# Performance work log

Measured on AMD Instinct MI355X. Metric: run time of the kernel, lower is better.

The kernel has to match this reference:

```python
import jax, jax.numpy as jnp
import numpy as np

N_NODES = 50000
N_EDGES = 800000
EPS = 1e-5

def _xavier(key, shape):
    fan_in, fan_out = shape[1], shape[0]
    lim = float(np.sqrt(6.0 / (fan_in + fan_out)))
    return jax.random.uniform(key, shape, jnp.float32, -lim, lim)

def setup_inputs() -> dict:
    key = jax.random.key(0)
    ks = jax.random.split(key, 12)
    x = jax.random.normal(ks[0], (N_NODES, 166), jnp.float32)
    edge_index = jax.random.randint(ks[1], (2, N_EDGES), 0, N_NODES, jnp.int32)
    dims = [(256, 166), (128, 256), (64, 128)]
    inp = {"x": x, "edge_index": edge_index}
    # SAGEConv layers: lin_l (applied to aggregated neighbors, has bias) and lin_r (self)
    names = ["1", "2", "e"]
    for i, (nm, (do, di)) in enumerate(zip(names, dims)):
        inp[f"Wl{nm}"] = _xavier(ks[2 + 2 * i], (do, di))
        inp[f"Wr{nm}"] = _xavier(ks[3 + 2 * i], (do, di))
        inp[f"b{nm}"] = jnp.zeros((do,), jnp.float32)
    # BatchNorm params for the two hidden conv layers
    inp["g1"] = jnp.ones((256,), jnp.float32); inp["bt1"] = jnp.zeros((256,), jnp.float32)
    inp["g2"] = jnp.ones((128,), jnp.float32); inp["bt2"] = jnp.zeros((128,), jnp.float32)
    # classifier
    inp["Wc"] = _xavier(ks[8], (2, 64))
    inp["bc"] = jnp.zeros((2,), jnp.float32)
    return inp

def _sage_conv(x, src, dst, Wl, Wr, b):
    # mean aggregation of source features at destination nodes
    agg = jax.ops.segment_sum(x[src], dst, num_segments=N_NODES)  # [N, d]
    deg = jax.ops.segment_sum(jnp.ones((src.shape[0],), x.dtype), dst, num_segments=N_NODES)
    agg = agg / jnp.maximum(deg, 1.0)[:, None]
    return agg @ Wl.T + x @ Wr.T + b

def _bn(x, g, b):
    m = jnp.mean(x, axis=0)
    v = jnp.var(x, axis=0)
    return (x - m) * jax.lax.rsqrt(v + EPS) * g + b

def reference(x, edge_index, Wl1, Wr1, b1, Wl2, Wr2, b2, Wle, Wre, be, g1, bt1, g2, bt2, Wc, bc):
    src, dst = edge_index[0], edge_index[1]
    h = _sage_conv(x, src, dst, Wl1, Wr1, b1)
    h = jax.nn.relu(_bn(h, g1, bt1))
    h = _sage_conv(h, src, dst, Wl2, Wr2, b2)
    h = jax.nn.relu(_bn(h, g2, bt2))
    embeddings = _sage_conv(h, src, dst, Wle, Wre, be)  # [N, 64]
    logits = embeddings @ Wc.T + bc  # [N, 2]
    return (logits, embeddings)
```

## Files before the change

kernel.cpp:

```cpp
#include <hip/hip_runtime.h>

#define NN 50000
#define NE 800000
#define NB 256
#define BNODES ((NN + NB - 1) / NB)
#define CAP 4096
#define BPART_BLKS ((NE + 8191) / 8192)
#define PREP_BLKS ((NN * 112 + 255) / 256)
#define PACK_BLKS ((180224 + 255) / 256)
static constexpr float BN_EPS = 1e-5f;

typedef __attribute__((ext_vector_type(8))) short bf16x8;
typedef __attribute__((ext_vector_type(4))) float f32x4;

__device__ inline unsigned short f2bf(float f) {
  unsigned int u = __float_as_uint(f);
  return (unsigned short)((u + 0x7FFFu + ((u >> 16) & 1u)) >> 16);
}
__device__ inline float bf2f(unsigned int h) { return __uint_as_float(h << 16); }
__device__ inline void gl_lds16(const char* g, char* l) {
  __builtin_amdgcn_global_load_lds((const __attribute__((address_space(1))) void*)g,
                                   (__attribute__((address_space(3))) void*)l, 16, 0, 0);
}

__device__ void dev_bpart(int bb, const int* __restrict__ src, const int* __restrict__ dst,
                          int* __restrict__ bcur, uint2* __restrict__ pairs) {
  __shared__ int cnt[NB], lbase[NB], lcur[NB];
  int t = threadIdx.x;
  cnt[t] = 0;
  __syncthreads();
  int e0 = bb * 8192 + t;
#pragma unroll
  for (int i = 0; i < 32; ++i) {
    int e = e0 + i * 256;
    if (e < NE) atomicAdd(&cnt[dst[e] / BNODES], 1);
  }
  __syncthreads();
  lbase[t] = cnt[t] ? (t * CAP + atomicAdd(&bcur[t], cnt[t])) : 0;
  lcur[t] = 0;
  __syncthreads();
#pragma unroll
  for (int i = 0; i < 32; ++i) {
    int e = e0 + i * 256;
    if (e < NE) {
      int d = dst[e];
      int b = d / BNODES;
      int p = atomicAdd(&lcur[b], 1);
      pairs[(size_t)lbase[b] + p] = uint2{(unsigned)src[e], (unsigned)d};
    }
  }
}

__global__ void k_front(const int* __restrict__ src, const int* __restrict__ dst,
                        int* __restrict__ bcur, uint2* __restrict__ pairs,
                        const float* __restrict__ x, unsigned int* __restrict__ xbu,
                        unsigned int* __restrict__ aggX,
                        const float* __restrict__ Wl1, const float* __restrict__ Wr1,
                        const float* __restrict__ Wl2, const float* __restrict__ Wr2,
                        const float* __restrict__ Wle, const float* __restrict__ Wre,
                        unsigned short* __restrict__ w1c, unsigned short* __restrict__ w2s,
                        unsigned short* __restrict__ w3s,
                        float* __restrict__ bnacc) {
  int b = blockIdx.x;
  if (b < BPART_BLKS) {
    dev_bpart(b, src, dst, bcur, pairs);
    return;
  }
  b -= BPART_BLKS;
  if (b < PREP_BLKS) {
    int i = b * 256 + threadIdx.x;
    if (i >= NN * 112) return;
    int r = i / 112, q = i - r * 112;
    if (q < 84) {
      int c0 = 2 * q, c1 = c0 + 1;
      float v0 = (c0 < 166) ? x[(size_t)r * 166 + c0] : 0.f;
      float v1 = (c1 < 166) ? x[(size_t)r * 166 + c1] : 0.f;
      xbu[(size_t)r * 96 + q] = (unsigned)f2bf(v0) | ((unsigned)f2bf(v1) << 16);
    } else if (q < 96) {
      xbu[(size_t)r * 96 + q] = 0u;
    } else if (q < 109) {
      aggX[(size_t)r * 96 + 83 + (q - 96)] = 0u;
    }
    return;
  }
  b -= PREP_BLKS;
  if (b < PACK_BLKS) {
    int idx = b * 256 + threadIdx.x;
    if (idx < 98304) {
      int n = idx / 384, k = idx - n * 384;
      float v = 0.f;
      if (k < 166) v = Wl1[(size_t)n * 166 + k];
      else if (k >= 192 && k < 358) v = Wr1[(size_t)n * 166 + (k - 192)];
      w1c[idx] = f2bf(v);
    } else if (idx < 163840) {
      int j = idx - 98304;
      int n = j / 256, k = j - n * 256;
      w2s[j] = f2bf(n < 128 ? Wl2[(size_t)n * 256 + k] : Wr2[(size_t)(n - 128) * 256 + k]);
    } else if (idx < 180224) {
      int j = idx - 163840;
      int n = j / 128, k = j - n * 128;
      w3s[j] = f2bf(n < 64 ? Wle[(size_t)n * 128 + k] : Wre[(size_t)(n - 64) * 128 + k]);
    }
    return;
  }
  int z = (b - PACK_BLKS) * 256 + threadIdx.x;
  if (z < 1024) bnacc[z] = 0.f;
}

__global__ void k_bscatter(const uint2* __restrict__ pairs, const int* __restrict__ bcur,
                           int2* __restrict__ begend, int* __restrict__ col) {
  __shared__ int dcnt[NB], ts[NB], doff[NB], dcur[NB];
  int t = threadIdx.x;
  int b = blockIdx.x;
  int n0 = b * BNODES;
  int ncnt = min(NN - n0, BNODES);
  int e0 = b * CAP, e1 = e0 + bcur[b];
  dcnt[t] = 0;
  __syncthreads();
  for (int e = e0 + t; e < e1; e += 256) atomicAdd(&dcnt[pairs[e].y - n0], 1);
  __syncthreads();
  ts[t] = dcnt[t];
  __syncthreads();
#pragma unroll
  for (int off = 1; off < NB; off <<= 1) {
    int u = (t >= off) ? ts[t - off] : 0;
    __syncthreads();
    ts[t] += u;
    __syncthreads();
  }
  doff[t] = ts[t] - dcnt[t];
  dcur[t] = 0;
  if (t < ncnt) begend[n0 + t] = int2{e0 + doff[t], e0 + doff[t] + dcnt[t]};
  __syncthreads();
  for (int e = e0 + t; e < e1; e += 256) {
    uint2 pr = pairs[e];
    int ld = pr.y - n0;
    int p = atomicAdd(&dcur[ld], 1);
    col[e0 + doff[ld] + p] = (int)pr.x;
  }
}

template <int D, int U, bool FUSE, bool OUTBF, bool CLS>
__global__ __launch_bounds__(256) void k_aggb(
    const unsigned int* __restrict__ feat, int fsu,
    const int2* __restrict__ begend, const int* __restrict__ col,
    const unsigned int* __restrict__ self, int ssu,
    const float* __restrict__ bias,
    void* __restrict__ outv, int osu,
    const float* __restrict__ Wc, const float* __restrict__ bc,
    float* __restrict__ logits) {
  constexpr int D2 = D / 2;
  constexpr int LPN = (D2 < 64) ? D2 : 64;
  constexpr int NPB = 256 / LPN;
  constexpr int C = (D2 + LPN - 1) / LPN;
  int node = blockIdx.x * NPB + threadIdx.x / LPN;
  if (node >= NN) return;
  int lane = threadIdx.x % LPN;
  int2 be = begend[node];
  int beg = be.x, end = be.y;
  float ax[C], ay[C];
#pragma unroll
  for (int c = 0; c < C; ++c) { ax[c] = 0.f; ay[c] = 0.f; }

  int j = beg;
  for (; j + U <= end; j += U) {
    const unsigned int* fp[U];
#pragma unroll
    for (int u = 0; u < U; ++u) fp[u] = feat + (size_t)col[j + u] * fsu;
#pragma unroll
    for (int c = 0; c < C; ++c) {
      int p = lane + c * LPN;
      unsigned int t[U];
#pragma unroll
      for (int u = 0; u < U; ++u) t[u] = (p < D2) ? fp[u][p] : 0u;
#pragma unroll
      for (int u = 0; u < U; ++u) {
        ax[c] += bf2f(t[u] & 0xffffu);
        ay[c] += bf2f(t[u] >> 16);
      }
    }
  }
  for (; j < end; ++j) {
    const unsigned int* fr = feat + (size_t)col[j] * fsu;
#pragma unroll
    for (int c = 0; c < C; ++c) {
      int p = lane + c * LPN;
      if (p < D2) {
        unsigned int t = fr[p];
        ax[c] += bf2f(t & 0xffffu);
        ay[c] += bf2f(t >> 16);
      }
    }
  }
  float inv = 1.0f / fmaxf((float)(end - beg), 1.0f);
  float s0 = 0.f, s1 = 0.f;
#pragma unroll
  for (int c = 0; c < C; ++c) {
    int p = lane + c * LPN;
    if (p < D2) {
      float vx = ax[c] * inv, vy = ay[c] * inv;
      if constexpr (FUSE) {
        unsigned int s = self[(size_t)node * ssu + p];
        vx += bf2f(s & 0xffffu) + bias[2 * p];
        vy += bf2f(s >> 16) + bias[2 * p + 1];
      }
      if constexpr (OUTBF) {
        unsigned int o = (unsigned int)f2bf(vx) | ((unsigned int)f2bf(vy) << 16);
        ((unsigned int*)outv)[(size_t)node * osu + p] = o;
      } else {
        float2 o{vx, vy};
        *reinterpret_cast<float2*>((float*)outv + (size_t)node * osu + 2 * p) = o;
      }
      if constexpr (CLS) {
        s0 += vx * Wc[2 * p] + vy * Wc[2 * p + 1];
        s1 += vx * Wc[64 + 2 * p] + vy * Wc[64 + 2 * p + 1];
      }
    }
  }
  if constexpr (CLS) {
#pragma unroll
    for (int m = 1; m < LPN; m <<= 1) {
      s0 += __shfl_xor(s0, m);
      s1 += __shfl_xor(s1, m);
    }
    if (lane == 0) {
      logits[node * 2 + 0] = s0 + bc[0];
      logits[node * 2 + 1] = s1 + bc[1];
    }
  }
}

template <bool BIASED, bool STATS>
__global__ __launch_bounds__(256) void k_gemm_mfma(
    const unsigned short* __restrict__ A0, const unsigned short* __restrict__ A1,
    int K1, int Astride, int KC,
    const unsigned short* __restrict__ W,
    const float* __restrict__ bias,
    unsigned short* __restrict__ out, int Ntot,
    float* __restrict__ statacc) {
  __shared__ __align__(16) char lds[65536];
  int tid = threadIdx.x;
  int lane = tid & 63;
  int w = tid >> 6;
  int wr = w >> 1, wc = w & 1;
  int m0 = blockIdx.x * 128;
  int n0 = blockIdx.y * 128;

  int srow = lane >> 3;
  int scol = (lane & 7) << 4;
  int ssw = scol ^ (srow << 4);
  const char* Wb = (const char*)W;

  f32x4 acc[4][4];
#pragma unroll
  for (int i = 0; i < 4; ++i)
#pragma unroll
    for (int j = 0; j < 4; ++j) acc[i][j] = f32x4{0.f, 0.f, 0.f, 0.f};

  auto stage = [&](int buf, int k0) {
    const char* Ab = (const char*)(k0 < K1 ? A0 : A1);
    int koff = k0 < K1 ? k0 : k0 - K1;
    char* dst = lds + buf * 32768 + w * 4096;
#pragma unroll
    for (int i = 0; i < 4; ++i) {
      int row = w * 32 + i * 8 + srow;
      int ga = m0 + row;
      ga = ga < NN ? ga : NN - 1;
      gl_lds16(Ab + ((size_t)ga * Astride + koff) * 2 + ssw, dst + i * 1024);
      gl_lds16(Wb + ((size_t)(n0 + row) * KC + k0) * 2 + ssw, dst + 16384 + i * 1024);
    }
  };
  auto compute = [&](int buf) {
    char* lA = lds + buf * 32768;
    char* lB = lA + 16384;
#pragma unroll
    for (int ks = 0; ks < 2; ++ks) {
      bf16x8 af[4], bfr[4];
      int ac = ks * 64 + ((lane >> 4) << 4);
#pragma unroll
      for (int f = 0; f < 4; ++f) {
        int ar = wr * 64 + f * 16 + (lane & 15);
        af[f] = *reinterpret_cast<const bf16x8*>(lA + ar * 128 + (ac ^ ((ar & 7) << 4)));
        int br = wc * 64 + f * 16 + (lane & 15);
        bfr[f] = *reinterpret_cast<const bf16x8*>(lB + br * 128 + (ac ^ ((br & 7) << 4)));
      }
#pragma unroll
      for (int fm = 0; fm < 4; ++fm)
#pragma unroll
        for (int fn = 0; fn < 4; ++fn)
          acc[fm][fn] = __builtin_amdgcn_mfma_f32_16x16x32_bf16(af[fm], bfr[fn], acc[fm][fn], 0, 0, 0);
    }
  };

  int nt = KC >> 6;
  stage(0, 0);
  if (nt > 1) stage(1, 64);
  for (int t = 0; t < nt - 1; ++t) {
    asm volatile("s_waitcnt vmcnt(8)" ::: "memory");
    __builtin_amdgcn_s_barrier();
    compute(t & 1);
    __builtin_amdgcn_s_barrier();
    if (t + 2 < nt) stage(t & 1, (t + 2) << 6);
  }
  asm volatile("s_waitcnt vmcnt(0)" ::: "memory");
  __builtin_amdgcn_s_barrier();
  compute((nt - 1) & 1);

  int nbase = n0 + wc * 64 + (lane & 15);
  float bv[4] = {0.f, 0.f, 0.f, 0.f};
  if constexpr (BIASED) {
#pragma unroll
    for (int fn = 0; fn < 4; ++fn) bv[fn] = bias[nbase + fn * 16];
  }
  float ssum[4] = {0.f, 0.f, 0.f, 0.f}, sqs[4] = {0.f, 0.f, 0.f, 0.f};
#pragma unroll
  for (int fm = 0; fm < 4; ++fm) {
    int mbase = m0 + wr * 64 + fm * 16 + ((lane >> 4) << 2);
#pragma unroll
    for (int j = 0; j < 4; ++j) {
      int m = mbase + j;
      if (m < NN) {
#pragma unroll
        for (int fn = 0; fn < 4; ++fn) {
          float v = acc[fm][fn][j] + bv[fn];
          out[(size_t)m * Ntot + nbase + fn * 16] = f2bf(v);
          if constexpr (STATS) { ssum[fn] += v; sqs[fn] += v * v; }
        }
      }
    }
  }
  if constexpr (STATS) {
#pragma unroll
    for (int fn = 0; fn < 4; ++fn) {
      float s = ssum[fn], q = sqs[fn];
      s += __shfl_xor(s, 16); s += __shfl_xor(s, 32);
      q += __shfl_xor(q, 16); q += __shfl_xor(q, 32);
      if (lane < 16) {
        atomicAdd(&statacc[nbase + fn * 16], s);
        atomicAdd(&statacc[Ntot + nbase + fn * 16], q);
      }
    }
  }
}

__global__ __launch_bounds__(256) void k_gemm_bn(
    const unsigned short* __restrict__ A, const float* __restrict__ scsh,
    const unsigned short* __restrict__ W,
    unsigned short* __restrict__ out, int KC, int Ntot) {
  __shared__ __align__(16) char lds[65536];
  int tid = threadIdx.x;
  int lane = tid & 63;
  int w = tid >> 6;
  int wr = w >> 1, wc = w & 1;
  int m0 = blockIdx.x * 128;
  int n0 = blockIdx.y * 128;

  int srow = lane >> 3;
  int cb = (lane & 7) << 4;
  int ssw = cb ^ (srow << 4);
  int kk0 = (lane & 7) << 3;
  const char* Wb = (const char*)W;

  f32x4 acc[4][4];
#pragma unroll
  for (int i = 0; i < 4; ++i)
#pragma unroll
    for (int j = 0; j < 4; ++j) acc[i][j] = f32x4{0.f, 0.f, 0.f, 0.f};

  uint4 areg[4];
  float4 sc[4];

  auto loadA = [&](int k0) {
    int kk = k0 + kk0;
    const float4* sp = (const float4*)(scsh + 2 * kk);
    sc[0] = sp[0]; sc[1] = sp[1]; sc[2] = sp[2]; sc[3] = sp[3];
#pragma unroll
    for (int i = 0; i < 4; ++i) {
      int row = w * 32 + i * 8 + srow;
      int ga = m0 + row;
      ga = ga < NN ? ga : NN - 1;
      areg[i] = *reinterpret_cast<const uint4*>(A + (size_t)ga * KC + kk);
    }
  };
  auto writeA = [&](int buf) {
    char* dstb = lds + buf * 32768;
#pragma unroll
    for (int i = 0; i < 4; ++i) {
      int row = w * 32 + i * 8 + srow;
      uint4 v = areg[i], o;
      float a, b;
      a = fmaxf(bf2f(v.x & 0xffffu) * sc[0].x + sc[0].y, 0.f);
      b = fmaxf(bf2f(v.x >> 16)     * sc[0].z + sc[0].w, 0.f);
      o.x = (unsigned)f2bf(a) | ((unsigned)f2bf(b) << 16);
      a = fmaxf(bf2f(v.y & 0xffffu) * sc[1].x + sc[1].y, 0.f);
      b = fmaxf(bf2f(v.y >> 16)     * sc[1].z + sc[1].w, 0.f);
      o.y = (unsigned)f2bf(a) | ((unsigned)f2bf(b) << 16);
      a = fmaxf(bf2f(v.z & 0xffffu) * sc[2].x + sc[2].y, 0.f);
      b = fmaxf(bf2f(v.z >> 16)     * sc[2].z + sc[2].w, 0.f);
      o.z = (unsigned)f2bf(a) | ((unsigned)f2bf(b) << 16);
      a = fmaxf(bf2f(v.w & 0xffffu) * sc[3].x + sc[3].y, 0.f);
      b = fmaxf(bf2f(v.w >> 16)     * sc[3].z + sc[3].w, 0.f);
      o.w = (unsigned)f2bf(a) | ((unsigned)f2bf(b) << 16);
      *reinterpret_cast<uint4*>(dstb + row * 128 + (cb ^ ((row & 7) << 4))) = o;
    }
  };
  auto stageW = [&](int buf, int k0) {
    char* dst = lds + buf * 32768 + 16384 + w * 4096;
#pragma unroll
    for (int i = 0; i < 4; ++i) {
      int row = w * 32 + i * 8 + srow;
      gl_lds16(Wb + ((size_t)(n0 + row) * KC + k0) * 2 + ssw, dst + i * 1024);
    }
  };
  auto compute = [&](int buf) {
    char* lA = lds + buf * 32768;
    char* lB = lA + 16384;
#pragma unroll
    for (int ks = 0; ks < 2; ++ks) {
      bf16x8 af[4], bfr[4];
      int ac = ks * 64 + ((lane >> 4) << 4);
#pragma unroll
      for (int f = 0; f < 4; ++f) {
        int ar = wr * 64 + f * 16 + (lane & 15);
        af[f] = *reinterpret_cast<const bf16x8*>(lA + ar * 128 + (ac ^ ((ar & 7) << 4)));
        int br = wc * 64 + f * 16 + (lane & 15);
        bfr[f] = *reinterpret_cast<const bf16x8*>(lB + br * 128 + (ac ^ ((br & 7) << 4)));
      }
#pragma unroll
      for (int fm = 0; fm < 4; ++fm)
#pragma unroll
        for (int fn = 0; fn < 4; ++fn)
          acc[fm][fn] = __builtin_amdgcn_mfma_f32_16x16x32_bf16(af[fm], bfr[fn], acc[fm][fn], 0, 0, 0);
    }
  };

  int nt = KC >> 6;
  loadA(0);
  stageW(0, 0);
  writeA(0);
  __syncthreads();
  int cur = 0;
  for (int t = 0; t < nt; ++t) {
    if (t + 1 < nt) { loadA((t + 1) << 6); stageW(cur ^ 1, (t + 1) << 6); }
    compute(cur);
    __syncthreads();
    if (t + 1 < nt) writeA(cur ^ 1);
    __syncthreads();
    cur ^= 1;
  }

  int nbase = n0 + wc * 64 + (lane & 15);
#pragma unroll
  for (int fm = 0; fm < 4; ++fm) {
    int mbase = m0 + wr * 64 + fm * 16 + ((lane >> 4) << 2);
#pragma unroll
    for (int j = 0; j < 4; ++j) {
      int m = mbase + j;
      if (m < NN) {
#pragma unroll
        for (int fn = 0; fn < 4; ++fn)
          out[(size_t)m * Ntot + nbase + fn * 16] = f2bf(acc[fm][fn][j]);
      }
    }
  }
}

template <int N, bool BF>
__global__ __launch_bounds__(256) void k_bn_stats2(const void* __restrict__ hv,
                                                   float* __restrict__ acc) {
  constexpr int CP = N / 2;
  constexpr int RG = 256 / CP;
  int cp = threadIdx.x % CP, rg = threadIdx.x / CP;
  int rpb = (NN + gridDim.x - 1) / gridDim.x;
  int r0 = blockIdx.x * rpb, r1 = min(r0 + rpb, NN);
  float s0 = 0.f, s1 = 0.f, q0 = 0.f, q1 = 0.f;
  for (int r = r0 + rg; r < r1; r += RG) {
    float v0, v1;
    if constexpr (BF) {
      unsigned int u = ((const unsigned int*)hv)[(size_t)r * CP + cp];
      v0 = bf2f(u & 0xffffu); v1 = bf2f(u >> 16);
    } else {
      float2 u = ((const float2*)hv)[(size_t)r * CP + cp];
      v0 = u.x; v1 = u.y;
    }
    s0 += v0; s1 += v1; q0 += v0 * v0; q1 += v1 * v1;
  }
  __shared__ float l0[256], l1[256], l2[256], l3[256];
  l0[threadIdx.x] = s0; l1[threadIdx.x] = s1; l2[threadIdx.x] = q0; l3[threadIdx.x] = q1;
  __syncthreads();
  if (rg == 0) {
#pragma unroll
    for (int g = 1; g < RG; ++g) {
      s0 += l0[g * CP + cp]; s1 += l1[g * CP + cp];
      q0 += l2[g * CP + cp]; q1 += l3[g * CP + cp];
    }
    atomicAdd(&acc[2 * cp], s0);
    atomicAdd(&acc[2 * cp + 1], s1);
    atomicAdd(&acc[N + 2 * cp], q0);
    atomicAdd(&acc[N + 2 * cp + 1], q1);
  }
}

template <int N>
__global__ void k_scsh(const float* __restrict__ acc, const float* __restrict__ g,
                       const float* __restrict__ b, float* __restrict__ scsh) {
  int c = threadIdx.x;
  float mean = acc[c] * (1.0f / NN);
  float var = acc[N + c] * (1.0f / NN) - mean * mean;
  float sc = g[c] * rsqrtf(var + BN_EPS);
  scsh[2 * c] = sc;
  scsh[2 * c + 1] = b[c] - mean * sc;
}

extern "C" void kernel_launch(void* const* d_in, const int* in_sizes, int n_in,
                              void* d_out, int out_size, void* d_ws, size_t ws_size,
                              hipStream_t stream) {
  const float* x   = (const float*)d_in[0];
  const int* ei    = (const int*)d_in[1];
  const float* Wl1 = (const float*)d_in[2];
  const float* Wr1 = (const float*)d_in[3];
  const float* b1  = (const float*)d_in[4];
  const float* Wl2 = (const float*)d_in[5];
  const float* Wr2 = (const float*)d_in[6];
  const float* b2  = (const float*)d_in[7];
  const float* Wle = (const float*)d_in[8];
  const float* Wre = (const float*)d_in[9];
  const float* be  = (const float*)d_in[10];
  const float* g1  = (const float*)d_in[11];
  const float* bt1 = (const float*)d_in[12];
  const float* g2  = (const float*)d_in[13];
  const float* bt2 = (const float*)d_in[14];
  const float* Wc  = (const float*)d_in[15];
  const float* bc  = (const float*)d_in[16];

  const int* src = ei;
  const int* dst = ei + NE;

  char* ws = (char*)d_ws;
  size_t off = 0;
  auto take = [&](size_t bytes) -> char* {
    char* p = ws + off;
    off = (off + bytes + 255) & ~(size_t)255;
    return p;
  };
  int* bkt_cur   = (int*)take(1024);
  float* bnacc1  = (float*)take(2048);
  float* bnacc2  = (float*)take(2048);
  float* scsh1   = (float*)take(512 * 4);
  float* scsh2   = (float*)take(256 * 4);
  int2* begend   = (int2*)take((size_t)NN * 8);
  uint2* pairs   = (uint2*)take((size_t)NB * CAP * 8);
  int* col       = (int*)take((size_t)NB * CAP * 4);
  unsigned short* w1c = (unsigned short*)take((size_t)256 * 384 * 2);
  unsigned short* w2s = (unsigned short*)take((size_t)256 * 256 * 2);
  unsigned short* w3s = (unsigned short*)take((size_t)128 * 128 * 2);
  unsigned int* xbu  = (unsigned int*)take((size_t)NN * 96 * 4);
  unsigned int* aggX = (unsigned int*)take((size_t)NN * 96 * 4);
  char* P1 = take((size_t)NN * 256 * 2);
  char* P0 = take((size_t)NN * 256 * 2);

  unsigned short* h1raw = (unsigned short*)P1;
  unsigned short* z2    = (unsigned short*)P0;
  unsigned short* h2raw = (unsigned short*)P1;
  unsigned short* z3    = (unsigned short*)P0;

  float* logits = (float*)d_out;
  float* emb    = (float*)d_out + (size_t)NN * 2;

  hipMemsetAsync(bkt_cur, 0, 1024, stream);

  {
    int grid = BPART_BLKS + PREP_BLKS + PACK_BLKS + 4;
    k_front<<<grid, 256, 0, stream>>>(src, dst, bkt_cur, pairs, x, xbu, aggX,
                                      Wl1, Wr1, Wl2, Wr2, Wle, Wre, w1c, w2s, w3s, bnacc1);
  }
  k_bscatter<<<NB, NB, 0, stream>>>(pairs, bkt_cur, begend, col);

  k_aggb<166, 4, false, true, false><<<(NN + 3) / 4, 256, 0, stream>>>(
      xbu, 96, begend, col, nullptr, 0, nullptr, aggX, 96, nullptr, nullptr, nullptr);
  {
    dim3 g((NN + 127) / 128, 2);
    k_gemm_mfma<true, true><<<g, 256, 0, stream>>>(
        (const unsigned short*)aggX, (const unsigned short*)xbu, 192, 192, 384,
        w1c, b1, h1raw, 256, bnacc1);
  }
  k_scsh<256><<<1, 256, 0, stream>>>(bnacc1, g1, bt1, scsh1);

  {
    dim3 g((NN + 127) / 128, 2);
    k_gemm_bn<<<g, 256, 0, stream>>>(h1raw, scsh1, w2s, z2, 256, 256);
  }
  k_aggb<128, 8, true, true, false><<<(NN + 3) / 4, 256, 0, stream>>>(
      (const unsigned int*)z2, 128, begend, col, (const unsigned int*)z2 + 64, 128, b2,
      h2raw, 64, nullptr, nullptr, nullptr);
  k_bn_stats2<128, true><<<512, 256, 0, stream>>>(h2raw, bnacc2);
  k_scsh<128><<<1, 128, 0, stream>>>(bnacc2, g2, bt2, scsh2);

  {
    dim3 g((NN + 127) / 128, 1);
    k_gemm_bn<<<g, 256, 0, stream>>>(h2raw, scsh2, w3s, z3, 128, 128);
  }
  k_aggb<64, 8, true, false, true><<<(NN + 7) / 8, 256, 0, stream>>>(
      (const unsigned int*)z3, 64, begend, col, (const unsigned int*)z3 + 32, 64, be,
      emb, 64, Wc, bc, logits);
}
```

Before: 274.0 us.

## Fold BN scale/shift into GEMM prologue and vectorize input prep

Drops the two single-block k_scsh launches. Each k_gemm_bn thread now computes the BatchNorm scale and shift directly from the accumulated sums, gamma and beta while loading A tiles. The x-to-bf16 prep is rewritten so each thread handles 8 columns with float2 loads and a uint4 store, with 32 threads per row instead of 112. This removes launch overhead and serialization gaps, at the cost of redundant rsqrt work and extra small loads inside the GEMM k-loop.

```diff
diff --git a/kernel.cpp b/kernel.cpp
--- a/kernel.cpp
+++ b/kernel.cpp
@@ -6,7 +6,7 @@
 #define BNODES ((NN + NB - 1) / NB)
 #define CAP 4096
 #define BPART_BLKS ((NE + 8191) / 8192)
-#define PREP_BLKS ((NN * 112 + 255) / 256)
+#define PREP_BLKS ((NN * 32 + 255) / 256)
 #define PACK_BLKS ((180224 + 255) / 256)
 static constexpr float BN_EPS = 1e-5f;
 
@@ -69,17 +69,26 @@
   b -= BPART_BLKS;
   if (b < PREP_BLKS) {
     int i = b * 256 + threadIdx.x;
-    if (i >= NN * 112) return;
-    int r = i / 112, q = i - r * 112;
-    if (q < 84) {
-      int c0 = 2 * q, c1 = c0 + 1;
-      float v0 = (c0 < 166) ? x[(size_t)r * 166 + c0] : 0.f;
-      float v1 = (c1 < 166) ? x[(size_t)r * 166 + c1] : 0.f;
-      xbu[(size_t)r * 96 + q] = (unsigned)f2bf(v0) | ((unsigned)f2bf(v1) << 16);
-    } else if (q < 96) {
-      xbu[(size_t)r * 96 + q] = 0u;
-    } else if (q < 109) {
-      aggX[(size_t)r * 96 + 83 + (q - 96)] = 0u;
+    int r = i >> 5, q = i & 31;
+    if (r >= NN) return;
+    if (q < 24) {
+      uint4 o = {0u, 0u, 0u, 0u};
+      if (q < 21) {
+        const float* xp = x + (size_t)r * 166 + 8 * q;
+        unsigned int* ou = (unsigned int*)&o;
+#pragma unroll
+        for (int j = 0; j < 4; ++j) {
+          int c = 8 * q + 2 * j;
+          if (c + 1 < 166) {
+            float2 v = *reinterpret_cast<const float2*>(xp + 2 * j);
+            ou[j] = (unsigned)f2bf(v.x) | ((unsigned)f2bf(v.y) << 16);
+          }
+        }
+      }
+      reinterpret_cast<uint4*>(xbu)[(size_t)r * 24 + q] = o;
+    } else if (q < 28) {
+      int j = q - 24;
+      reinterpret_cast<uint4*>(aggX)[(size_t)r * 24 + 20 + j] = uint4{0u, 0u, 0u, 0u};
     }
     return;
   }
@@ -344,7 +353,9 @@
 }
 
 __global__ __launch_bounds__(256) void k_gemm_bn(
-    const unsigned short* __restrict__ A, const float* __restrict__ scsh,
+    const unsigned short* __restrict__ A,
+    const float* __restrict__ bnacc, const float* __restrict__ gamma,
+    const float* __restrict__ beta, int Nbn,
     const unsigned short* __restrict__ W,
     unsigned short* __restrict__ out, int KC, int Ntot) {
   __shared__ __align__(16) char lds[65536];
@@ -372,8 +383,14 @@
 
   auto loadA = [&](int k0) {
     int kk = k0 + kk0;
-    const float4* sp = (const float4*)(scsh + 2 * kk);
-    sc[0] = sp[0]; sc[1] = sp[1]; sc[2] = sp[2]; sc[3] = sp[3];
+#pragma unroll
+    for (int u = 0; u < 4; ++u) {
+      int c0 = kk + 2 * u, c1 = c0 + 1;
+      float m0f = bnacc[c0] * (1.0f / NN), m1f = bnacc[c1] * (1.0f / NN);
+      float s0 = gamma[c0] * rsqrtf(bnacc[Nbn + c0] * (1.0f / NN) - m0f * m0f + BN_EPS);
+      float s1 = gamma[c1] * rsqrtf(bnacc[Nbn + c1] * (1.0f / NN) - m1f * m1f + BN_EPS);
+      sc[u] = float4{s0, beta[c0] - m0f * s0, s1, beta[c1] - m1f * s1};
+    }
 #pragma unroll
     for (int i = 0; i < 4; ++i) {
       int row = w * 32 + i * 8 + srow;
@@ -499,17 +516,6 @@
     atomicAdd(&acc[N + 2 * cp], q0);
     atomicAdd(&acc[N + 2 * cp + 1], q1);
   }
-}
-
-template <int N>
-__global__ void k_scsh(const float* __restrict__ acc, const float* __restrict__ g,
-                       const float* __restrict__ b, float* __restrict__ scsh) {
-  int c = threadIdx.x;
-  float mean = acc[c] * (1.0f / NN);
-  float var = acc[N + c] * (1.0f / NN) - mean * mean;
-  float sc = g[c] * rsqrtf(var + BN_EPS);
-  scsh[2 * c] = sc;
-  scsh[2 * c + 1] = b[c] - mean * sc;
 }
 
 extern "C" void kernel_launch(void* const* d_in, const int* in_sizes, int n_in,
@@ -546,8 +552,6 @@
   int* bkt_cur   = (int*)take(1024);
   float* bnacc1  = (float*)take(2048);
   float* bnacc2  = (float*)take(2048);
-  float* scsh1   = (float*)take(512 * 4);
-  float* scsh2   = (float*)take(256 * 4);
   int2* begend   = (int2*)take((size_t)NN * 8);
   uint2* pairs   = (uint2*)take((size_t)NB * CAP * 8);
   int* col       = (int*)take((size_t)NB * CAP * 4);
@@ -584,21 +588,19 @@
         (const unsigned short*)aggX, (const unsigned short*)xbu, 192, 192, 384,
         w1c, b1, h1raw, 256, bnacc1);
   }
-  k_scsh<256><<<1, 256, 0, stream>>>(bnacc1, g1, bt1, scsh1);
 
   {
     dim3 g((NN + 127) / 128, 2);
-    k_gemm_bn<<<g, 256, 0, stream>>>(h1raw, scsh1, w2s, z2, 256, 256);
+    k_gemm_bn<<<g, 256, 0, stream>>>(h1raw, bnacc1, g1, bt1, 256, w2s, z2, 256, 256);
   }
   k_aggb<128, 8, true, true, false><<<(NN + 3) / 4, 256, 0, stream>>>(
       (const unsigned int*)z2, 128, begend, col, (const unsigned int*)z2 + 64, 128, b2,
       h2raw, 64, nullptr, nullptr, nullptr);
   k_bn_stats2<128, true><<<512, 256, 0, stream>>>(h2raw, bnacc2);
-  k_scsh<128><<<1, 128, 0, stream>>>(bnacc2, g2, bt2, scsh2);
 
   {
     dim3 g((NN + 127) / 128, 1);
-    k_gemm_bn<<<g, 256, 0, stream>>>(h2raw, scsh2, w3s, z3, 128, 128);
+    k_gemm_bn<<<g, 256, 0, stream>>>(h2raw, bnacc2, g2, bt2, 128, w3s, z3, 128, 128);
   }
   k_aggb<64, 8, true, false, true><<<(NN + 7) / 8, 256, 0, stream>>>(
       (const unsigned int*)z3, 64, begend, col, (const unsigned int*)z3 + 32, 64, be,
```

Result: no change. 272.7 us (-0.5%).
